# Kernel tuning notes

Hardware: AMD Instinct MI355X
Metric: run time of the kernel (lower is better)

Reference implementation:

```python
import jax, jax.numpy as jnp
import numpy as np

N = 16384           # nodes
E = 131072          # edges per graph (avg degree 16)
D_BODY = 2048
D_FACE = 512
H = 32              # hidden width (encoder / GCN)
BN_EPS = 1e-5


def _batchnorm(x, gamma, beta):
    # BatchNorm1d in training mode: biased batch stats over the node/batch dim
    mu = jnp.mean(x, axis=0)
    var = jnp.var(x, axis=0)
    return (x - mu) * jax.lax.rsqrt(var + BN_EPS) * gamma + beta


def _prelu(x, a):
    return jnp.where(x > 0, x, a * x)


def _gcn(x, feats, src, dst, W, b, n):
    # Edge weight = ReLU(cosine similarity of raw feats); GCN symmetric norm with self loops.
    fn = feats * jax.lax.rsqrt(jnp.sum(feats * feats, axis=1, keepdims=True) + 1e-12)
    sim = jax.nn.relu(jnp.sum(fn[src] * fn[dst], axis=1))        # [E]
    loop = jnp.arange(n)
    s = jnp.concatenate([src, loop])
    d = jnp.concatenate([dst, loop])
    w = jnp.concatenate([sim, jnp.ones((n,), x.dtype)])
    deg = jax.ops.segment_sum(w, d, num_segments=n)              # weighted in-degree
    dn = jax.lax.rsqrt(jnp.clip(deg, 1e-6))
    coef = dn[s] * dn[d] * w                                     # [E+N]
    agg = jax.ops.segment_sum(x[s] * coef[:, None], d, num_segments=n)  # [N,H]
    return agg @ W + b


def setup_inputs() -> dict:
    key = jax.random.key(0)
    ks = jax.random.split(key, 20)
    inp = {
        "x": jax.random.normal(ks[0], (N, 2), jnp.float32),
        "body_feats": jax.random.normal(ks[1], (N, D_BODY), jnp.float32),
        "face_feats": jax.random.normal(ks[2], (N, D_FACE), jnp.float32),
        "edge_index_body": jax.random.randint(ks[3], (2, E), 0, N),
        "edge_index_face": jax.random.randint(ks[4], (2, E), 0, N),
        # encoder: Linear(2,32) -> BN(32) -> PReLU -> Dropout(0) -> Linear(32,32)
        "enc_w1": jax.random.normal(ks[5], (2, H), jnp.float32) * 0.5,
        "enc_b1": jnp.zeros((H,), jnp.float32),
        "bn_gamma": jnp.ones((H,), jnp.float32),
        "bn_beta": jnp.zeros((H,), jnp.float32),
        "prelu_a": jnp.float32(0.25),
        "enc_w2": jax.random.normal(ks[6], (H, H), jnp.float32) * 0.18,
        "enc_b2": jnp.zeros((H,), jnp.float32),
        "w0_w": jax.random.normal(ks[7], (H, 1), jnp.float32) * 0.18,
        "w0_b": jnp.zeros((1,), jnp.float32),
        "gcnb_w": jax.random.normal(ks[8], (H, H), jnp.float32) * 0.18,
        "gcnb_b": jnp.zeros((H,), jnp.float32),
        "gcnf_w": jax.random.normal(ks[9], (H, H), jnp.float32) * 0.18,
        "gcnf_b": jnp.zeros((H,), jnp.float32),
        "wb_w": jax.random.normal(ks[10], (H, 1), jnp.float32) * 0.18,
        "wb_b": jnp.zeros((1,), jnp.float32),
        "wf_w": jax.random.normal(ks[11], (H, 1), jnp.float32) * 0.18,
        "wf_b": jnp.zeros((1,), jnp.float32),
    }
    return inp


def reference(x, body_feats, face_feats, edge_index_body, edge_index_face,
              enc_w1, enc_b1, bn_gamma, bn_beta, prelu_a, enc_w2, enc_b2,
              w0_w, w0_b, gcnb_w, gcnb_b, gcnf_w, gcnf_b, wb_w, wb_b, wf_w, wf_b):
    n = x.shape[0]
    h = _prelu(_batchnorm(x @ enc_w1 + enc_b1, bn_gamma, bn_beta), prelu_a)
    emb = h @ enc_w2 + enc_b2                                    # [N,32]
    xb = _gcn(emb, body_feats, edge_index_body[0], edge_index_body[1], gcnb_w, gcnb_b, n)
    xf = _gcn(emb, face_feats, edge_index_face[0], edge_index_face[1], gcnf_w, gcnf_b, n)
    lin = (emb @ w0_w + w0_b)[:, 0]
    sb = (xb @ wb_w + wb_b)[:, 0]
    sf = (xf @ wf_w + wf_b)[:, 0]
    return lin + sb + sf                                          # [N]
```

## Files before the change

### kernel.cpp

```cpp
#include <hip/hip_runtime.h>
#include <hip/hip_fp16.h>

#define N_NODES 16384
#define N_EDGES 131072
#define DB 2048
#define DF 512
#define FP8_SCALE 16.0f
#define FP8_DESCALE (1.0f / 256.0f)
#define SPREAD 16
#define BUCKET 64

#define WS_STATS   0
#define WS_PAR     320
#define WS_DNB     576
#define WS_DNF     (WS_DNB + N_NODES)
#define WS_WQB     (WS_DNF + N_NODES)
#define WS_WQF     (WS_WQB + N_NODES)
#define WS_CNTB    (WS_WQF + N_NODES)
#define WS_CNTF    (WS_CNTB + N_NODES * SPREAD)
#define WS_EDGEB   (WS_CNTF + N_NODES * SPREAD)
#define WS_EDGEF   (WS_EDGEB + N_NODES * BUCKET)
#define WS_FNB     (WS_EDGEF + N_NODES * BUCKET)
#define WS_FNF     (WS_FNB + N_NODES * DB / 4)

typedef float fv2 __attribute__((ext_vector_type(2)));

#if __has_builtin(__builtin_amdgcn_cvt_pk_f32_fp8) && __has_builtin(__builtin_amdgcn_cvt_pk_fp8_f32)
#define HAS_FP8HW 1
#else
#define HAS_FP8HW 0
#endif

__device__ __forceinline__ uint16_t f2h_bits(float f) {
    union { __half h; uint16_t u; } c; c.h = __float2half_rn(f); return c.u;
}
__device__ __forceinline__ float h_bits2f(uint16_t u) {
    union { uint16_t u; __half h; } c; c.u = u; return __half2float(c.h);
}

#if !HAS_FP8HW
__device__ __forceinline__ float fp8d_soft(uint32_t b) {
    uint32_t s = (b >> 7) & 1u, e = (b >> 3) & 0xFu, m = b & 7u;
    float v = (e == 0) ? (float)m * 0.001953125f
                       : (1.0f + (float)m * 0.125f) * exp2f((float)((int)e - 7));
    return s ? -v : v;
}
__device__ __forceinline__ uint32_t fp8e_soft(float f) {
    uint32_t s = (__float_as_uint(f) >> 31) << 7;
    float a = fabsf(f);
    if (a < 0.015625f) {
        int m = (int)rintf(a * 512.0f);
        if (m > 7) return s | (1u << 3);
        return s | (uint32_t)m;
    }
    uint32_t u = __float_as_uint(a);
    uint32_t r = u + 0x000FFFFFu + ((u >> 20) & 1u);
    int e8 = (int)(r >> 23) - 127 + 7;
    if (e8 >= 16) return s | (15u << 3) | 6u;
    return s | ((uint32_t)e8 << 3) | ((r >> 20) & 7u);
}
#endif

__device__ __forceinline__ float u32dot(uint32_t u, const float* s, float acc) {
#if HAS_FP8HW
    fv2 lo = __builtin_amdgcn_cvt_pk_f32_fp8(u, false);
    fv2 hi = __builtin_amdgcn_cvt_pk_f32_fp8(u, true);
    acc += s[0] * lo.x; acc += s[1] * lo.y;
    acc += s[2] * hi.x; acc += s[3] * hi.y;
#else
    acc += s[0] * fp8d_soft(u & 0xFF);
    acc += s[1] * fp8d_soft((u >> 8) & 0xFF);
    acc += s[2] * fp8d_soft((u >> 16) & 0xFF);
    acc += s[3] * fp8d_soft((u >> 24) & 0xFF);
#endif
    return acc;
}
__device__ __forceinline__ void u32cvt(uint32_t u, float* d) {
#if HAS_FP8HW
    fv2 lo = __builtin_amdgcn_cvt_pk_f32_fp8(u, false);
    fv2 hi = __builtin_amdgcn_cvt_pk_f32_fp8(u, true);
    d[0] = lo.x; d[1] = lo.y; d[2] = hi.x; d[3] = hi.y;
#else
    d[0] = fp8d_soft(u & 0xFF); d[1] = fp8d_soft((u >> 8) & 0xFF);
    d[2] = fp8d_soft((u >> 16) & 0xFF); d[3] = fp8d_soft((u >> 24) & 0xFF);
#endif
}
__device__ __forceinline__ uint32_t pack4_fp8(float a, float b, float c, float d) {
#if HAS_FP8HW
    uint32_t u = 0;
    u = __builtin_amdgcn_cvt_pk_fp8_f32(a, b, u, false);
    u = __builtin_amdgcn_cvt_pk_fp8_f32(c, d, u, true);
    return u;
#else
    return fp8e_soft(a) | (fp8e_soft(b) << 8) | (fp8e_soft(c) << 16) | (fp8e_soft(d) << 24);
#endif
}
__device__ __forceinline__ float dot16_fp8(uint4 r, const float* s, float acc) {
    acc = u32dot(r.x, s + 0, acc);  acc = u32dot(r.y, s + 4, acc);
    acc = u32dot(r.z, s + 8, acc);  acc = u32dot(r.w, s + 12, acc);
    return acc;
}

__global__ void k_pre(const float* __restrict__ x, float* __restrict__ ws) {
    if (blockIdx.x < 64) {
        float s0 = 0.f, s1 = 0.f, s2 = 0.f, s3 = 0.f, s4 = 0.f;
        for (int i = blockIdx.x * 256 + threadIdx.x; i < N_NODES; i += 64 * 256) {
            float2 v = ((const float2*)x)[i];
            s0 += v.x; s1 += v.y;
            s2 += v.x * v.x; s3 += v.y * v.y; s4 += v.x * v.y;
        }
        #pragma unroll
        for (int off = 32; off; off >>= 1) {
            s0 += __shfl_down(s0, off); s1 += __shfl_down(s1, off);
            s2 += __shfl_down(s2, off); s3 += __shfl_down(s3, off);
            s4 += __shfl_down(s4, off);
        }
        __shared__ float red[4][5];
        int w = threadIdx.x >> 6;
        if ((threadIdx.x & 63) == 0) {
            red[w][0] = s0; red[w][1] = s1; red[w][2] = s2; red[w][3] = s3; red[w][4] = s4;
        }
        __syncthreads();
        if (threadIdx.x < 5) {
            ws[WS_STATS + blockIdx.x * 5 + threadIdx.x] =
                red[0][threadIdx.x] + red[1][threadIdx.x] +
                red[2][threadIdx.x] + red[3][threadIdx.x];
        }
    } else {
        int j = (blockIdx.x - 64) * 256 + threadIdx.x;
        ((int*)(ws + WS_CNTB))[j] = 0;
    }
}

__global__ void k_scatnorm(const int* __restrict__ eib, const int* __restrict__ eif,
                           const float* __restrict__ bfeat, const float* __restrict__ ffeat,
                           const float* __restrict__ w1, const float* __restrict__ b1,
                           const float* __restrict__ gamma, const float* __restrict__ beta,
                           const float* __restrict__ w2, const float* __restrict__ b2,
                           const float* __restrict__ w0w, const float* __restrict__ w0b,
                           const float* __restrict__ gbw, const float* __restrict__ gbb,
                           const float* __restrict__ gfw, const float* __restrict__ gfb,
                           const float* __restrict__ wbw, const float* __restrict__ wbb,
                           const float* __restrict__ wfw, const float* __restrict__ wfb,
                           float* __restrict__ ws) {
    __shared__ float redf[4];
    int b = blockIdx.x;
    if (b == 0) {
        __shared__ float st5[5];
        if (threadIdx.x < 5) {
            float t = 0.f;
            for (int k = 0; k < 64; k++) t += ws[WS_STATS + k * 5 + threadIdx.x];
            st5[threadIdx.x] = t;
        }
        __syncthreads();
        const float inv_n = 1.0f / (float)N_NODES;
        float m0 = st5[0] * inv_n, m1 = st5[1] * inv_n;
        float v0 = st5[2] * inv_n - m0 * m0;
        float v1 = st5[3] * inv_n - m1 * m1;
        float cv = st5[4] * inv_n - m0 * m1;
        float* par = ws + WS_PAR;
        int j = threadIdx.x;
        if (j < 32) {
            float W0 = w1[j], W1 = w1[32 + j];
            float mu  = m0 * W0 + m1 * W1 + b1[j];
            float var = W0 * W0 * v0 + W1 * W1 * v1 + 2.f * W0 * W1 * cv;
            float is  = rsqrtf(var + 1e-5f) * gamma[j];
            par[j]      = W0 * is;
            par[32 + j] = W1 * is;
            par[64 + j] = (b1[j] - mu) * is + beta[j];
            float u0 = 0.f, ub = 0.f, uf = 0.f;
            for (int k = 0; k < 32; k++) {
                float w2jk = w2[j * 32 + k];
                float vbk = 0.f, vfk = 0.f;
                for (int n = 0; n < 32; n++) {
                    vbk += gbw[k * 32 + n] * wbw[n];
                    vfk += gfw[k * 32 + n] * wfw[n];
                }
                u0 += w2jk * w0w[k];
                ub += w2jk * vbk;
                uf += w2jk * vfk;
            }
            par[96 + j]  = u0;
            par[128 + j] = ub;
            par[160 + j] = uf;
        }
        if (threadIdx.x == 0) {
            float C = w0b[0] + wbb[0] + wfb[0];
            float pc0 = 0.f, pcb = 0.f, pcf = 0.f;
            for (int k = 0; k < 32; k++) {
                float vbk = 0.f, vfk = 0.f;
                for (int n = 0; n < 32; n++) {
                    vbk += gbw[k * 32 + n] * wbw[n];
                    vfk += gfw[k * 32 + n] * wfw[n];
                }
                pc0 += b2[k] * w0w[k];
                pcb += b2[k] * vbk;
                pcf += b2[k] * vfk;
                C   += gbb[k] * wbw[k] + gfb[k] * wfw[k];
            }
            par[192] = C; par[193] = pc0; par[194] = pcb; par[195] = pcf;
        }
    } else if (b <= 1024) {
        int e = (b - 1) * 256 + threadIdx.x;
        if (e < N_EDGES) {
            int s = eib[e], d = eib[N_EDGES + e];
            int pos = atomicAdd(&((int*)(ws + WS_CNTB))[d * SPREAD], 1);
            if (pos < BUCKET)
                ((uint32_t*)(ws + WS_EDGEB))[d * BUCKET + pos] = (uint32_t)s;
        } else {
            int e2 = e - N_EDGES;
            int s = eif[e2], d = eif[N_EDGES + e2];
            int pos = atomicAdd(&((int*)(ws + WS_CNTF))[d * SPREAD], 1);
            if (pos < BUCKET)
                ((uint32_t*)(ws + WS_EDGEF))[d * BUCKET + pos] = (uint32_t)s;
        }
    } else if (b <= 1024 + N_NODES) {
        int row = b - 1025;
        int t = threadIdx.x;
        const float4* F = (const float4*)bfeat + (size_t)row * (DB / 4);
        float4 a0 = F[2 * t];
        float4 a1 = F[2 * t + 1];
        float aa = a0.x * a0.x + a0.y * a0.y + a0.z * a0.z + a0.w * a0.w
                 + a1.x * a1.x + a1.y * a1.y + a1.z * a1.z + a1.w * a1.w;
        #pragma unroll
        for (int off = 32; off; off >>= 1) aa += __shfl_xor(aa, off);
        if ((t & 63) == 0) redf[t >> 6] = aa;
        __syncthreads();
        float tot = redf[0] + redf[1] + redf[2] + redf[3];
        float inv = rsqrtf(tot + 1e-12f) * FP8_SCALE;
        uint2 o;
        o.x = pack4_fp8(a0.x * inv, a0.y * inv, a0.z * inv, a0.w * inv);
        o.y = pack4_fp8(a1.x * inv, a1.y * inv, a1.z * inv, a1.w * inv);
        ((uint2*)(ws + WS_FNB))[(size_t)row * 256 + t] = o;
    } else {
        int idx = (b - 1025 - N_NODES) * 4 + (threadIdx.x >> 6);
        int lane = threadIdx.x & 63;
        if (idx >= N_NODES) return;
        const float4* F = (const float4*)ffeat + (size_t)idx * (DF / 4);
        float4 a0 = F[2 * lane];
        float4 a1 = F[2 * lane + 1];
        float aa = a0.x * a0.x + a0.y * a0.y + a0.z * a0.z + a0.w * a0.w
                 + a1.x * a1.x + a1.y * a1.y + a1.z * a1.z + a1.w * a1.w;
        #pragma unroll
        for (int off = 32; off; off >>= 1) aa += __shfl_xor(aa, off);
        float inv = rsqrtf(aa + 1e-12f) * FP8_SCALE;
        uint2 o;
        o.x = pack4_fp8(a0.x * inv, a0.y * inv, a0.z * inv, a0.w * inv);
        o.y = pack4_fp8(a1.x * inv, a1.y * inv, a1.z * inv, a1.w * inv);
        ((uint2*)(ws + WS_FNF))[(size_t)idx * 64 + lane] = o;
    }
}

__device__ __forceinline__ float wave_p(const float* __restrict__ par, float2 v,
                                        float alpha, int coef_base, int lane) {
    int j = lane & 31;
    float z = v.x * par[j] + v.y * par[32 + j] + par[64 + j];
    float h = z > 0.f ? z : alpha * z;
    float p = h * par[coef_base + j];
    #pragma unroll
    for (int off = 16; off; off >>= 1) p += __shfl_xor(p, off);
    return p;
}

__global__ void k_edge_all(const float* __restrict__ x, const float* __restrict__ prelu_a,
                           float* __restrict__ ws) {
    int wid  = (int)((blockIdx.x * blockDim.x + threadIdx.x) >> 6);
    int lane = threadIdx.x & 63;
    const float* par = ws + WS_PAR;
    if (wid < N_NODES) {
        uint32_t* edges = (uint32_t*)(ws + WS_EDGEB) + wid * BUCKET;
        int cnt = ((const int*)(ws + WS_CNTB))[wid * SPREAD];
        int en = cnt < BUCKET ? cnt : BUCKET;
        float wdeg = 0.f;
        if (en > 0) {
            const uint4* fn = (const uint4*)(ws + WS_FNB);
            const uint4* Dp = fn + (size_t)wid * 128;
            uint4 r0 = Dp[lane], r1 = Dp[lane + 64];
            float dstf[32];
            u32cvt(r0.x, dstf + 0);  u32cvt(r0.y, dstf + 4);
            u32cvt(r0.z, dstf + 8);  u32cvt(r0.w, dstf + 12);
            u32cvt(r1.x, dstf + 16); u32cvt(r1.y, dstf + 20);
            u32cvt(r1.z, dstf + 24); u32cvt(r1.w, dstf + 28);
            int i = 0;
            for (; i + 3 < en; i += 4) {
                uint32_t w[4];
                uint4 lo[4], hi[4];
                #pragma unroll
                for (int k = 0; k < 4; k++) w[k] = edges[i + k];
                #pragma unroll
                for (int k = 0; k < 4; k++) {
                    const uint4* P = fn + (size_t)(w[k] & 0xFFFFu) * 128;
                    lo[k] = P[lane]; hi[k] = P[lane + 64];
                }
                float s[4];
                #pragma unroll
                for (int k = 0; k < 4; k++)
                    s[k] = dot16_fp8(hi[k], dstf + 16, dot16_fp8(lo[k], dstf, 0.f));
                #pragma unroll
                for (int off = 32; off; off >>= 1) {
                    #pragma unroll
                    for (int k = 0; k < 4; k++) s[k] += __shfl_xor(s[k], off);
                }
                if (lane == 0) {
                    #pragma unroll
                    for (int k = 0; k < 4; k++) {
                        float m = fmaxf(s[k], 0.f) * FP8_DESCALE;
                        edges[i + k] = (w[k] & 0xFFFFu) | ((uint32_t)f2h_bits(m) << 16);
                        wdeg += m;
                    }
                }
            }
            for (; i < en; i++) {
                uint32_t w0 = edges[i];
                const uint4* A = fn + (size_t)(w0 & 0xFFFFu) * 128;
                uint4 a0 = A[lane], a1 = A[lane + 64];
                float s0 = dot16_fp8(a1, dstf + 16, dot16_fp8(a0, dstf, 0.f));
                #pragma unroll
                for (int off = 32; off; off >>= 1) s0 += __shfl_xor(s0, off);
                if (lane == 0) {
                    float m0 = fmaxf(s0, 0.f) * FP8_DESCALE;
                    edges[i] = (w0 & 0xFFFFu) | ((uint32_t)f2h_bits(m0) << 16);
                    wdeg += m0;
                }
            }
        }
        float2 v = ((const float2*)x)[wid];
        float pb = wave_p(par, v, prelu_a[0], 128, lane);
        if (lane == 0) {
            float dn = rsqrtf(fmaxf(1.f + wdeg, 1e-6f));
            ws[WS_DNB + wid] = dn;
            ws[WS_WQB + wid] = dn * (par[194] + pb);
        }
    } else {
        int nid = wid - N_NODES;
        if (nid >= N_NODES) return;
        uint32_t* edges = (uint32_t*)(ws + WS_EDGEF) + nid * BUCKET;
        int cnt = ((const int*)(ws + WS_CNTF))[nid * SPREAD];
        int en = cnt < BUCKET ? cnt : BUCKET;
        float wdeg = 0.f;
        if (en > 0) {
            const uint2* fn = (const uint2*)(ws + WS_FNF);
            uint2 sv = fn[(size_t)nid * 64 + lane];
            float dstf[8];
            u32cvt(sv.x, dstf); u32cvt(sv.y, dstf + 4);
            int i = 0;
            for (; i + 3 < en; i += 4) {
                uint32_t w0 = edges[i], w1 = edges[i + 1], w2 = edges[i + 2], w3 = edges[i + 3];
                uint2 r0 = fn[(size_t)(w0 & 0xFFFFu) * 64 + lane];
                uint2 r1 = fn[(size_t)(w1 & 0xFFFFu) * 64 + lane];
                uint2 r2 = fn[(size_t)(w2 & 0xFFFFu) * 64 + lane];
                uint2 r3 = fn[(size_t)(w3 & 0xFFFFu) * 64 + lane];
                float c0 = u32dot(r0.y, dstf + 4, u32dot(r0.x, dstf, 0.f));
                float c1 = u32dot(r1.y, dstf + 4, u32dot(r1.x, dstf, 0.f));
                float c2 = u32dot(r2.y, dstf + 4, u32dot(r2.x, dstf, 0.f));
                float c3 = u32dot(r3.y, dstf + 4, u32dot(r3.x, dstf, 0.f));
                #pragma unroll
                for (int off = 32; off; off >>= 1) {
                    c0 += __shfl_xor(c0, off); c1 += __shfl_xor(c1, off);
                    c2 += __shfl_xor(c2, off); c3 += __shfl_xor(c3, off);
                }
                if (lane == 0) {
                    float m0 = fmaxf(c0, 0.f) * FP8_DESCALE;
                    float m1 = fmaxf(c1, 0.f) * FP8_DESCALE;
                    float m2 = fmaxf(c2, 0.f) * FP8_DESCALE;
                    float m3 = fmaxf(c3, 0.f) * FP8_DESCALE;
                    edges[i]     = (w0 & 0xFFFFu) | ((uint32_t)f2h_bits(m0) << 16);
                    edges[i + 1] = (w1 & 0xFFFFu) | ((uint32_t)f2h_bits(m1) << 16);
                    edges[i + 2] = (w2 & 0xFFFFu) | ((uint32_t)f2h_bits(m2) << 16);
                    edges[i + 3] = (w3 & 0xFFFFu) | ((uint32_t)f2h_bits(m3) << 16);
                    wdeg += m0 + m1 + m2 + m3;
                }
            }
            for (; i < en; i++) {
                uint32_t w0 = edges[i];
                uint2 r0 = fn[(size_t)(w0 & 0xFFFFu) * 64 + lane];
                float c0 = u32dot(r0.y, dstf + 4, u32dot(r0.x, dstf, 0.f));
                #pragma unroll
                for (int off = 32; off; off >>= 1) c0 += __shfl_xor(c0, off);
                if (lane == 0) {
                    float m0 = fmaxf(c0, 0.f) * FP8_DESCALE;
                    edges[i] = (w0 & 0xFFFFu) | ((uint32_t)f2h_bits(m0) << 16);
                    wdeg += m0;
                }
            }
        }
        float2 v = ((const float2*)x)[nid];
        float pf = wave_p(par, v, prelu_a[0], 160, lane);
        if (lane == 0) {
            float dn = rsqrtf(fmaxf(1.f + wdeg, 1e-6f));
            ws[WS_DNF + nid] = dn;
            ws[WS_WQF + nid] = dn * (par[195] + pf);
        }
    }
}

__global__ void k_out(const float* __restrict__ x, const float* __restrict__ prelu_a,
                      float* __restrict__ out, const float* __restrict__ ws) {
    __shared__ float part[128];
    int half = threadIdx.x >> 7;
    int li   = threadIdx.x & 127;
    int i    = blockIdx.x * 128 + li;
    int g = half;
    const float* par = ws + WS_PAR;
    const uint32_t* eg = (const uint32_t*)(ws + (g ? WS_EDGEF : WS_EDGEB)) + i * BUCKET;
    const float* wq    = ws + (g ? WS_WQF : WS_WQB);
    int cnt = ((const int*)(ws + (g ? WS_CNTF : WS_CNTB)))[i * SPREAD];
    int en = cnt < BUCKET ? cnt : BUCKET;
    float sum = 0.f;
    for (int e = 0; e < en; e++) {
        uint32_t w = eg[e];
        float sm = h_bits2f((uint16_t)(w >> 16));
        if (sm > 0.f) sum += sm * wq[w & 0xFFFFu];
    }
    float2 v = ((const float2*)x)[i];
    float alpha = prelu_a[0];
    float pv = g ? par[195] : par[194];
    float p0 = par[193] + par[192];
    #pragma unroll
    for (int j = 0; j < 32; j++) {
        float z = v.x * par[j] + v.y * par[32 + j] + par[64 + j];
        float h = z > 0.f ? z : alpha * z;
        pv += h * par[(g ? 160 : 128) + j];
        if (!g) p0 += h * par[96 + j];
    }
    float dn = ws[(g ? WS_DNF : WS_DNB) + i];
    float contrib = dn * dn * pv + dn * sum;
    if (half == 1) part[li] = contrib;
    __syncthreads();
    if (half == 0) out[i] = p0 + contrib + part[li];
}

extern "C" void kernel_launch(void* const* d_in, const int* in_sizes, int n_in,
                              void* d_out, int out_size, void* d_ws, size_t ws_size,
                              hipStream_t stream) {
    const float* x     = (const float*)d_in[0];
    const float* bfeat = (const float*)d_in[1];
    const float* ffeat = (const float*)d_in[2];
    const int*   eib   = (const int*)d_in[3];
    const int*   eif   = (const int*)d_in[4];
    const float* w1    = (const float*)d_in[5];
    const float* b1    = (const float*)d_in[6];
    const float* gam   = (const float*)d_in[7];
    const float* bet   = (const float*)d_in[8];
    const float* pa    = (const float*)d_in[9];
    const float* w2    = (const float*)d_in[10];
    const float* b2    = (const float*)d_in[11];
    const float* w0w   = (const float*)d_in[12];
    const float* w0b   = (const float*)d_in[13];
    const float* gbw   = (const float*)d_in[14];
    const float* gbb   = (const float*)d_in[15];
    const float* gfw   = (const float*)d_in[16];
    const float* gfb   = (const float*)d_in[17];
    const float* wbw   = (const float*)d_in[18];
    const float* wbb   = (const float*)d_in[19];
    const float* wfw   = (const float*)d_in[20];
    const float* wfb   = (const float*)d_in[21];

    float* ws  = (float*)d_ws;
    float* out = (float*)d_out;

    k_pre<<<dim3(64 + 2 * N_NODES * SPREAD / 256), dim3(256), 0, stream>>>(x, ws);
    k_scatnorm<<<dim3(1025 + N_NODES + N_NODES / 4), dim3(256), 0, stream>>>(
        eib, eif, bfeat, ffeat, w1, b1, gam, bet, w2, b2, w0w, w0b,
        gbw, gbb, gfw, gfb, wbw, wbb, wfw, wfb, ws);
    k_edge_all<<<dim3(2 * N_NODES / 4), dim3(256), 0, stream>>>(x, pa, ws);
    k_out<<<dim3(N_NODES / 128), dim3(256), 0, stream>>>(x, pa, out, ws);
}
```

Measured before the change: 142.9 us.

## Move feature normalization into pre kernel and parallelize parameter folding

The bandwidth-heavy row normalization and FP8 quantization of body and face features now run in the first kernel, alongside the BN stats and counter clearing, instead of in the scatter kernel. The scatter kernel shrinks to the parameter-folding block plus the edge bucketing blocks. The folding block now computes the GCN-weight times output-weight vectors once in parallel in shared memory instead of redundantly per thread. The aim is to rebalance work between launches and shorten the serial tail of block 0, at the cost of a larger first kernel.

New measurement: 121.7 us. 1.17x faster.

```diff
diff --git a/kernel.cpp b/kernel.cpp
--- a/kernel.cpp
+++ b/kernel.cpp
@@ -101,10 +101,13 @@
     return acc;
 }
 
-__global__ void k_pre(const float* __restrict__ x, float* __restrict__ ws) {
-    if (blockIdx.x < 64) {
+__global__ void k_pre(const float* __restrict__ x, const float* __restrict__ bfeat,
+                      const float* __restrict__ ffeat, float* __restrict__ ws) {
+    __shared__ float red[4][5];
+    int b = blockIdx.x;
+    if (b < 64) {
         float s0 = 0.f, s1 = 0.f, s2 = 0.f, s3 = 0.f, s4 = 0.f;
-        for (int i = blockIdx.x * 256 + threadIdx.x; i < N_NODES; i += 64 * 256) {
+        for (int i = b * 256 + threadIdx.x; i < N_NODES; i += 64 * 256) {
             float2 v = ((const float2*)x)[i];
             s0 += v.x; s1 += v.y;
             s2 += v.x * v.x; s3 += v.y * v.y; s4 += v.x * v.y;
@@ -115,42 +118,83 @@
             s2 += __shfl_down(s2, off); s3 += __shfl_down(s3, off);
             s4 += __shfl_down(s4, off);
         }
-        __shared__ float red[4][5];
         int w = threadIdx.x >> 6;
         if ((threadIdx.x & 63) == 0) {
             red[w][0] = s0; red[w][1] = s1; red[w][2] = s2; red[w][3] = s3; red[w][4] = s4;
         }
         __syncthreads();
         if (threadIdx.x < 5) {
-            ws[WS_STATS + blockIdx.x * 5 + threadIdx.x] =
+            ws[WS_STATS + b * 5 + threadIdx.x] =
                 red[0][threadIdx.x] + red[1][threadIdx.x] +
                 red[2][threadIdx.x] + red[3][threadIdx.x];
         }
+    } else if (b < 2112) {
+        int j = (b - 64) * 256 + threadIdx.x;
+        ((int*)(ws + WS_CNTB))[j] = 0;
+    } else if (b < 18496) {
+        int row = b - 2112;
+        int t = threadIdx.x;
+        const float4* F = (const float4*)bfeat + (size_t)row * (DB / 4);
+        float4 a0 = F[2 * t];
+        float4 a1 = F[2 * t + 1];
+        float aa = a0.x * a0.x + a0.y * a0.y + a0.z * a0.z + a0.w * a0.w
+                 + a1.x * a1.x + a1.y * a1.y + a1.z * a1.z + a1.w * a1.w;
+        #pragma unroll
+        for (int off = 32; off; off >>= 1) aa += __shfl_xor(aa, off);
+        if ((t & 63) == 0) red[t >> 6][0] = aa;
+        __syncthreads();
+        float tot = red[0][0] + red[1][0] + red[2][0] + red[3][0];
+        float inv = rsqrtf(tot + 1e-12f) * FP8_SCALE;
+        uint2 o;
+        o.x = pack4_fp8(a0.x * inv, a0.y * inv, a0.z * inv, a0.w * inv);
+        o.y = pack4_fp8(a1.x * inv, a1.y * inv, a1.z * inv, a1.w * inv);
+        ((uint2*)(ws + WS_FNB))[(size_t)row * 256 + t] = o;
     } else {
-        int j = (blockIdx.x - 64) * 256 + threadIdx.x;
-        ((int*)(ws + WS_CNTB))[j] = 0;
-    }
-}
-
-__global__ void k_scatnorm(const int* __restrict__ eib, const int* __restrict__ eif,
-                           const float* __restrict__ bfeat, const float* __restrict__ ffeat,
-                           const float* __restrict__ w1, const float* __restrict__ b1,
-                           const float* __restrict__ gamma, const float* __restrict__ beta,
-                           const float* __restrict__ w2, const float* __restrict__ b2,
-                           const float* __restrict__ w0w, const float* __restrict__ w0b,
-                           const float* __restrict__ gbw, const float* __restrict__ gbb,
-                           const float* __restrict__ gfw, const float* __restrict__ gfb,
-                           const float* __restrict__ wbw, const float* __restrict__ wbb,
-                           const float* __restrict__ wfw, const float* __restrict__ wfb,
-                           float* __restrict__ ws) {
-    __shared__ float redf[4];
+        int idx = (b - 18496) * 4 + (threadIdx.x >> 6);
+        int lane = threadIdx.x & 63;
+        if (idx >= N_NODES) return;
+        const float4* F = (const float4*)ffeat + (size_t)idx * (DF / 4);
+        float4 a0 = F[2 * lane];
+        float4 a1 = F[2 * lane + 1];
+        float aa = a0.x * a0.x + a0.y * a0.y + a0.z * a0.z + a0.w * a0.w
+                 + a1.x * a1.x + a1.y * a1.y + a1.z * a1.z + a1.w * a1.w;
+        #pragma unroll
+        for (int off = 32; off; off >>= 1) aa += __shfl_xor(aa, off);
+        float inv = rsqrtf(aa + 1e-12f) * FP8_SCALE;
+        uint2 o;
+        o.x = pack4_fp8(a0.x * inv, a0.y * inv, a0.z * inv, a0.w * inv);
+        o.y = pack4_fp8(a1.x * inv, a1.y * inv, a1.z * inv, a1.w * inv);
+        ((uint2*)(ws + WS_FNF))[(size_t)idx * 64 + lane] = o;
+    }
+}
+
+__global__ void k_scat(const int* __restrict__ eib, const int* __restrict__ eif,
+                       const float* __restrict__ w1, const float* __restrict__ b1,
+                       const float* __restrict__ gamma, const float* __restrict__ beta,
+                       const float* __restrict__ w2, const float* __restrict__ b2,
+                       const float* __restrict__ w0w, const float* __restrict__ w0b,
+                       const float* __restrict__ gbw, const float* __restrict__ gbb,
+                       const float* __restrict__ gfw, const float* __restrict__ gfb,
+                       const float* __restrict__ wbw, const float* __restrict__ wbb,
+                       const float* __restrict__ wfw, const float* __restrict__ wfb,
+                       float* __restrict__ ws) {
     int b = blockIdx.x;
     if (b == 0) {
         __shared__ float st5[5];
-        if (threadIdx.x < 5) {
-            float t = 0.f;
-            for (int k = 0; k < 64; k++) t += ws[WS_STATS + k * 5 + threadIdx.x];
-            st5[threadIdx.x] = t;
+        __shared__ float vb[32], vf[32];
+        int t = threadIdx.x;
+        if (t < 5) {
+            float s = 0.f;
+            for (int k = 0; k < 64; k++) s += ws[WS_STATS + k * 5 + t];
+            st5[t] = s;
+        }
+        if (t >= 64 && t < 128) {
+            int k = t & 31;
+            const float* gw = (t < 96) ? gbw : gfw;
+            const float* ww = (t < 96) ? wbw : wfw;
+            float v = 0.f;
+            for (int n = 0; n < 32; n++) v += gw[k * 32 + n] * ww[n];
+            if (t < 96) vb[k] = v; else vf[k] = v;
         }
         __syncthreads();
         const float inv_n = 1.0f / (float)N_NODES;
@@ -171,36 +215,26 @@
             float u0 = 0.f, ub = 0.f, uf = 0.f;
             for (int k = 0; k < 32; k++) {
                 float w2jk = w2[j * 32 + k];
-                float vbk = 0.f, vfk = 0.f;
-                for (int n = 0; n < 32; n++) {
-                    vbk += gbw[k * 32 + n] * wbw[n];
-                    vfk += gfw[k * 32 + n] * wfw[n];
-                }
                 u0 += w2jk * w0w[k];
-                ub += w2jk * vbk;
-                uf += w2jk * vfk;
+                ub += w2jk * vb[k];
+                uf += w2jk * vf[k];
             }
             par[96 + j]  = u0;
             par[128 + j] = ub;
             par[160 + j] = uf;
         }
-        if (threadIdx.x == 0) {
+        if (threadIdx.x == 32) {
             float C = w0b[0] + wbb[0] + wfb[0];
             float pc0 = 0.f, pcb = 0.f, pcf = 0.f;
             for (int k = 0; k < 32; k++) {
-                float vbk = 0.f, vfk = 0.f;
-                for (int n = 0; n < 32; n++) {
-                    vbk += gbw[k * 32 + n] * wbw[n];
-                    vfk += gfw[k * 32 + n] * wfw[n];
-                }
                 pc0 += b2[k] * w0w[k];
-                pcb += b2[k] * vbk;
-                pcf += b2[k] * vfk;
+                pcb += b2[k] * vb[k];
+                pcf += b2[k] * vf[k];
                 C   += gbb[k] * wbw[k] + gfb[k] * wfw[k];
             }
             par[192] = C; par[193] = pc0; par[194] = pcb; par[195] = pcf;
         }
-    } else if (b <= 1024) {
+    } else {
         int e = (b - 1) * 256 + threadIdx.x;
         if (e < N_EDGES) {
             int s = eib[e], d = eib[N_EDGES + e];
@@ -214,40 +248,6 @@
             if (pos < BUCKET)
                 ((uint32_t*)(ws + WS_EDGEF))[d * BUCKET + pos] = (uint32_t)s;
         }
-    } else if (b <= 1024 + N_NODES) {
-        int row = b - 1025;
-        int t = threadIdx.x;
-        const float4* F = (const float4*)bfeat + (size_t)row * (DB / 4);
-        float4 a0 = F[2 * t];
-        float4 a1 = F[2 * t + 1];
-        float aa = a0.x * a0.x + a0.y * a0.y + a0.z * a0.z + a0.w * a0.w
-                 + a1.x * a1.x + a1.y * a1.y + a1.z * a1.z + a1.w * a1.w;
-        #pragma unroll
-        for (int off = 32; off; off >>= 1) aa += __shfl_xor(aa, off);
-        if ((t & 63) == 0) redf[t >> 6] = aa;
-        __syncthreads();
-        float tot = redf[0] + redf[1] + redf[2] + redf[3];
-        float inv = rsqrtf(tot + 1e-12f) * FP8_SCALE;
-        uint2 o;
-        o.x = pack4_fp8(a0.x * inv, a0.y * inv, a0.z * inv, a0.w * inv);
-        o.y = pack4_fp8(a1.x * inv, a1.y * inv, a1.z * inv, a1.w * inv);
-        ((uint2*)(ws + WS_FNB))[(size_t)row * 256 + t] = o;
-    } else {
-        int idx = (b - 1025 - N_NODES) * 4 + (threadIdx.x >> 6);
-        int lane = threadIdx.x & 63;
-        if (idx >= N_NODES) return;
-        const float4* F = (const float4*)ffeat + (size_t)idx * (DF / 4);
-        float4 a0 = F[2 * lane];
-        float4 a1 = F[2 * lane + 1];
-        float aa = a0.x * a0.x + a0.y * a0.y + a0.z * a0.z + a0.w * a0.w
-                 + a1.x * a1.x + a1.y * a1.y + a1.z * a1.z + a1.w * a1.w;
-        #pragma unroll
-        for (int off = 32; off; off >>= 1) aa += __shfl_xor(aa, off);
-        float inv = rsqrtf(aa + 1e-12f) * FP8_SCALE;
-        uint2 o;
-        o.x = pack4_fp8(a0.x * inv, a0.y * inv, a0.z * inv, a0.w * inv);
-        o.y = pack4_fp8(a1.x * inv, a1.y * inv, a1.z * inv, a1.w * inv);
-        ((uint2*)(ws + WS_FNF))[(size_t)idx * 64 + lane] = o;
     }
 }
 
@@ -459,9 +459,9 @@
     float* ws  = (float*)d_ws;
     float* out = (float*)d_out;
 
-    k_pre<<<dim3(64 + 2 * N_NODES * SPREAD / 256), dim3(256), 0, stream>>>(x, ws);
-    k_scatnorm<<<dim3(1025 + N_NODES + N_NODES / 4), dim3(256), 0, stream>>>(
-        eib, eif, bfeat, ffeat, w1, b1, gam, bet, w2, b2, w0w, w0b,
+    k_pre<<<dim3(22592), dim3(256), 0, stream>>>(x, bfeat, ffeat, ws);
+    k_scat<<<dim3(1025), dim3(256), 0, stream>>>(
+        eib, eif, w1, b1, gam, bet, w2, b2, w0w, w0b,
         gbw, gbb, gfw, gfb, wbw, wbb, wfw, wfb, ws);
     k_edge_all<<<dim3(2 * N_NODES / 4), dim3(256), 0, stream>>>(x, pa, ws);
     k_out<<<dim3(N_NODES / 128), dim3(256), 0, stream>>>(x, pa, out, ws);
```
